# Performance work log

Measured on AMD Instinct MI355X. Metric: run time of the kernel, lower is better.

## Reference

```python
import jax, jax.numpy as jnp
import numpy as np
import math

V, D, H, KVH, L, T, B = 32000, 1024, 16, 4, 4, 2048, 2
HD = D // H            # head_dim = 64
GROUP = H // KVH       # GQA group size = 4
KVW = KVH * HD         # kv width = 256
EPS = 1e-5


def _alibi_slopes(n_heads):
    # n_heads=16 is a power of two
    start = 2.0 ** (-2.0 ** (-(math.log2(n_heads) - 3)))
    return np.array([start * start ** i for i in range(n_heads)], dtype=np.float32)


def setup_inputs() -> dict:
    key = jax.random.key(0)
    ks = jax.random.split(key, 8)
    s = 0.02
    inp = {
        "tok_emb": jax.random.normal(ks[0], (V, D), jnp.float32) * s,
        "ln1_s": jnp.ones((L, D), jnp.float32),
        "ln1_b": jnp.zeros((L, D), jnp.float32),
        "qkv_w": jax.random.normal(ks[1], (L, D, D + 2 * KVW), jnp.float32) * s,
        "qkv_b": jnp.zeros((L, D + 2 * KVW), jnp.float32),
        "proj_w": jax.random.normal(ks[2], (L, D, D), jnp.float32) * s,
        "proj_b": jnp.zeros((L, D), jnp.float32),
        "ln2_s": jnp.ones((L, D), jnp.float32),
        "ln2_b": jnp.zeros((L, D), jnp.float32),
        "fc1_w": jax.random.normal(ks[3], (L, D, 4 * D), jnp.float32) * s,
        "fc1_b": jnp.zeros((L, 4 * D), jnp.float32),
        "fc2_w": jax.random.normal(ks[4], (L, 4 * D, D), jnp.float32) * s,
        "fc2_b": jnp.zeros((L, D), jnp.float32),
        "lnf_s": jnp.ones((D,), jnp.float32),
        "lnf_b": jnp.zeros((D,), jnp.float32),
        "idx": jax.random.randint(ks[5], (B, T), 0, V, jnp.int32),
    }
    return inp


def _ln(x, s, b):
    mu = jnp.mean(x, axis=-1, keepdims=True)
    var = jnp.var(x, axis=-1, keepdims=True)
    return (x - mu) * jax.lax.rsqrt(var + EPS) * s + b


def _forward(tok_emb, ln1_s, ln1_b, qkv_w, qkv_b, proj_w, proj_b,
             ln2_s, ln2_b, fc1_w, fc1_b, fc2_w, fc2_b, lnf_s, lnf_b, idx):
    x = tok_emb[idx]  # (B, T, D); ALiBi => no learned positional embedding

    # combined causal mask + ALiBi bias: (1, H, T, T)
    slopes = jnp.asarray(_alibi_slopes(H)).reshape(1, H, 1, 1)
    pos = jnp.arange(T, dtype=jnp.float32)
    rel = jnp.minimum(pos[None, :] - pos[:, None], 0.0)  # (T, T), clamp_max(0)
    causal = pos[None, :] <= pos[:, None]
    bias = jnp.where(causal[None, None], rel[None, None] * slopes, -jnp.inf)

    scale = 1.0 / math.sqrt(HD)
    for l in range(L):
        h = _ln(x, ln1_s[l], ln1_b[l])
        qkv = h @ qkv_w[l] + qkv_b[l]
        q = qkv[..., :D].reshape(B, T, H, HD).transpose(0, 2, 1, 3)
        k = qkv[..., D:D + KVW].reshape(B, T, KVH, HD).transpose(0, 2, 1, 3)
        v = qkv[..., D + KVW:].reshape(B, T, KVH, HD).transpose(0, 2, 1, 3)
        k = jnp.repeat(k, GROUP, axis=1)  # GQA broadcast -> (B, H, T, HD)
        v = jnp.repeat(v, GROUP, axis=1)
        att = jnp.einsum("bhqd,bhkd->bhqk", q, k) * scale + bias
        att = jax.nn.softmax(att, axis=-1)
        o = jnp.einsum("bhqk,bhkd->bhqd", att, v)
        o = o.transpose(0, 2, 1, 3).reshape(B, T, D)
        x = x + o @ proj_w[l] + proj_b[l]
        h = _ln(x, ln2_s[l], ln2_b[l])
        x = x + jax.nn.gelu(h @ fc1_w[l] + fc1_b[l], approximate=False) @ fc2_w[l] + fc2_b[l]

    x = _ln(x, lnf_s, lnf_b)
    logits = x @ tok_emb.T  # tied head (no bias)
    return logits


def reference(tok_emb, ln1_s, ln1_b, qkv_w, qkv_b, proj_w, proj_b,
              ln2_s, ln2_b, fc1_w, fc1_b, fc2_w, fc2_b, lnf_s, lnf_b, idx):
    return _forward(tok_emb, ln1_s, ln1_b, qkv_w, qkv_b, proj_w, proj_b,
                    ln2_s, ln2_b, fc1_w, fc1_b, fc2_w, fc2_b, lnf_s, lnf_b, idx)
```

## Files before the change

### kernel.cpp

```cpp
#include <hip/hip_runtime.h>

#define DEV __device__ __forceinline__
typedef unsigned short u16;
typedef __bf16 bf16_t;
typedef bf16_t bf16x8 __attribute__((ext_vector_type(8)));
typedef float f32x4 __attribute__((ext_vector_type(4)));

DEV u16 f2bf(float f){ unsigned u=__float_as_uint(f); return (u16)((u + 0x7fffu + ((u>>16)&1u))>>16); }

DEV void gl_lds16(const void* g, void* l){
  __builtin_amdgcn_global_load_lds((__attribute__((address_space(1))) void*)g,
                                   (__attribute__((address_space(3))) void*)l, 16, 0, 0);
}
DEV f32x4 MFMA(bf16x8 a, bf16x8 b, f32x4 c){
  return __builtin_amdgcn_mfma_f32_16x16x32_bf16(a, b, c, 0, 0, 0);
}
DEV bf16x8 ld8(const u16* p){ return *(const bf16x8*)p; }

__global__ __launch_bounds__(256) void k_embed(const int* __restrict__ idx,
                                               const float* __restrict__ emb,
                                               float* __restrict__ x){
  int row = blockIdx.x;
  int tok = idx[row];
  const float4* s = (const float4*)(emb + (size_t)tok*1024);
  float4* d = (float4*)(x + (size_t)row*1024);
  d[threadIdx.x] = s[threadIdx.x];
}

__global__ __launch_bounds__(256) void k_ln(const float* __restrict__ x,
                                            const float* __restrict__ sc,
                                            const float* __restrict__ bi,
                                            u16* __restrict__ out){
  int row = blockIdx.x;
  const float* xr = x + (size_t)row*1024;
  float4 v = ((const float4*)xr)[threadIdx.x];
  float s = v.x+v.y+v.z+v.w;
  float q = v.x*v.x+v.y*v.y+v.z*v.z+v.w*v.w;
  #pragma unroll
  for(int m=1;m<64;m<<=1){ s += __shfl_xor(s,m); q += __shfl_xor(q,m); }
  __shared__ float ss[4], sq[4];
  int w = threadIdx.x>>6;
  if((threadIdx.x&63)==0){ ss[w]=s; sq[w]=q; }
  __syncthreads();
  s = ss[0]+ss[1]+ss[2]+ss[3];
  q = sq[0]+sq[1]+sq[2]+sq[3];
  float mu = s*(1.f/1024.f);
  float var = q*(1.f/1024.f) - mu*mu;
  float rs = rsqrtf(var + 1e-5f);
  float4 sv = ((const float4*)sc)[threadIdx.x];
  float4 bv = ((const float4*)bi)[threadIdx.x];
  ushort4 o;
  o.x = f2bf((v.x-mu)*rs*sv.x + bv.x);
  o.y = f2bf((v.y-mu)*rs*sv.y + bv.y);
  o.z = f2bf((v.z-mu)*rs*sv.z + bv.z);
  o.w = f2bf((v.w-mu)*rs*sv.w + bv.w);
  *(ushort4*)(out + (size_t)row*1024 + threadIdx.x*4) = o;
}

__global__ __launch_bounds__(256) void k_convT(const float* __restrict__ W,
                                               u16* __restrict__ Wt, int K, int N){
  __shared__ float tile[32][33];
  size_t loff = (size_t)blockIdx.z * K * N;
  W  += loff;  Wt += loff;
  int n0 = blockIdx.x*32, k0 = blockIdx.y*32;
  int tx = threadIdx.x & 31, ty = threadIdx.x >> 5;
  #pragma unroll
  for(int i=0;i<4;i++)
    tile[ty + i*8][tx] = W[(size_t)(k0 + ty + i*8)*N + n0 + tx];
  __syncthreads();
  #pragma unroll
  for(int i=0;i<4;i++)
    Wt[(size_t)(n0 + ty + i*8)*K + k0 + tx] = f2bf(tile[tx][ty + i*8]);
}

__global__ __launch_bounds__(256) void k_conv(const float* __restrict__ in,
                                              u16* __restrict__ out, int n4){
  int i = blockIdx.x*256 + threadIdx.x;
  if(i < n4){
    float4 v = ((const float4*)in)[i];
    ushort4 o; o.x=f2bf(v.x); o.y=f2bf(v.y); o.z=f2bf(v.z); o.w=f2bf(v.w);
    ((ushort4*)out)[i] = o;
  }
}

template<int EPI, int SWAP>
__global__ __launch_bounds__(256) void k_gemm(const u16* __restrict__ A,
                                              const u16* __restrict__ Bt,
                                              const float* __restrict__ bias,
                                              void* __restrict__ out,
                                              float* __restrict__ res,
                                              int M, int N, int K, int m_base){
  __shared__ __align__(16) u16 As[128*64];
  __shared__ __align__(16) u16 Bs[128*64];
  int t = threadIdx.x, l = t & 63, w = t >> 6;
  int g = l >> 4, lr = l & 15;
  int wr = w >> 1, wc = w & 1;
  int m0, n0;
  if constexpr(SWAP){ m0 = m_base + blockIdx.x*128; n0 = blockIdx.y*128; }
  else              { m0 = m_base + blockIdx.y*128; n0 = blockIdx.x*128; }
  f32x4 acc[4][4];
  #pragma unroll
  for(int i=0;i<4;i++)
    #pragma unroll
    for(int j=0;j<4;j++) acc[i][j] = f32x4{0.f,0.f,0.f,0.f};

  int sr = t >> 3;
  int sc = (((t & 7) ^ (sr & 7)) * 8);
  const u16* pa = A  + (size_t)(m0 + sr)*K + sc;
  const u16* pb = Bt + (size_t)(n0 + sr)*K + sc;
  u16* lda = As + t*8;
  u16* ldb = Bs + t*8;
  const int rs_a = (lr & 7)*8;

  for(int k0=0; k0<K; k0+=64){
    #pragma unroll
    for(int i=0;i<4;i++){
      gl_lds16(pa + (size_t)(i*32)*K, lda + i*2048);
      gl_lds16(pb + (size_t)(i*32)*K, ldb + i*2048);
    }
    pa += 64; pb += 64;
    __syncthreads();
    bf16x8 af[4][2], bfr[4][2];
    #pragma unroll
    for(int mi=0;mi<4;mi++){
      int row = wr*64 + mi*16 + lr;
      af[mi][0] = ld8(&As[row*64 + ((g*8     ) ^ rs_a)]);
      af[mi][1] = ld8(&As[row*64 + ((g*8 + 32) ^ rs_a)]);
    }
    #pragma unroll
    for(int ni=0;ni<4;ni++){
      int row = wc*64 + ni*16 + lr;
      bfr[ni][0] = ld8(&Bs[row*64 + ((g*8     ) ^ rs_a)]);
      bfr[ni][1] = ld8(&Bs[row*64 + ((g*8 + 32) ^ rs_a)]);
    }
    #pragma unroll
    for(int mi=0;mi<4;mi++)
      #pragma unroll
      for(int ni=0;ni<4;ni++){
        acc[mi][ni] = MFMA(af[mi][0], bfr[ni][0], acc[mi][ni]);
        acc[mi][ni] = MFMA(af[mi][1], bfr[ni][1], acc[mi][ni]);
      }
    __syncthreads();
  }

  float bv[4];
  #pragma unroll
  for(int ni=0;ni<4;ni++){
    if constexpr(EPI==3) bv[ni] = 0.f;
    else bv[ni] = bias[n0 + wc*64 + ni*16 + lr];
  }
  #pragma unroll
  for(int mi=0;mi<4;mi++){
    int row = m0 + wr*64 + mi*16 + g*4;
    #pragma unroll
    for(int ni=0;ni<4;ni++){
      int col = n0 + wc*64 + ni*16 + lr;
      #pragma unroll
      for(int r=0;r<4;r++){
        float v = acc[mi][ni][r] + bv[ni];
        size_t oidx = (size_t)(row + r)*N + col;
        if constexpr(EPI==0){
          ((u16*)out)[oidx] = f2bf(v);
        } else if constexpr(EPI==1){
          res[oidx] += v;
        } else if constexpr(EPI==2){
          float gv = 0.5f*v*(1.f + erff(v*0.70710678118654752f));
          ((u16*)out)[oidx] = f2bf(gv);
        } else {
          ((float*)out)[oidx] = v;
        }
      }
    }
  }
}

__global__ __launch_bounds__(256) void k_gemm_f32b(const u16* __restrict__ A,
                                                   const float* __restrict__ B,
                                                   float* __restrict__ out,
                                                   int M, int N, int K, int m_base){
  __shared__ __align__(16) u16 As[128*32];
  __shared__ __align__(16) u16 Bs[128*32];
  int t = threadIdx.x, l = t & 63, w = t >> 6;
  int g = l >> 4, lr = l & 15;
  int wr = w >> 1, wc = w & 1;
  int m0 = m_base + blockIdx.y*128, n0 = blockIdx.x*128;
  f32x4 acc[4][4];
  #pragma unroll
  for(int i=0;i<4;i++)
    #pragma unroll
    for(int j=0;j<4;j++) acc[i][j] = f32x4{0.f,0.f,0.f,0.f};

  int r0 = t >> 2, c0 = (t & 3)*8;
  const u16* pa0 = A + (size_t)(m0 + r0)*K + c0;
  const u16* pa1 = A + (size_t)(m0 + r0 + 64)*K + c0;
  u16* la0 = As + t*8;  u16* la1 = As + (t+256)*8;
  int br = t >> 1, bc = (t & 1)*16;
  const float* pb = B + (size_t)(n0 + br)*K + bc;

  for(int k0=0; k0<K; k0+=32){
    gl_lds16(pa0, la0); gl_lds16(pa1, la1);
    pa0 += 32; pa1 += 32;
    float4 f0 = ((const float4*)pb)[0];
    float4 f1 = ((const float4*)pb)[1];
    float4 f2 = ((const float4*)pb)[2];
    float4 f3 = ((const float4*)pb)[3];
    pb += 32;
    ushort4 u0{f2bf(f0.x),f2bf(f0.y),f2bf(f0.z),f2bf(f0.w)};
    ushort4 u1{f2bf(f1.x),f2bf(f1.y),f2bf(f1.z),f2bf(f1.w)};
    ushort4 u2{f2bf(f2.x),f2bf(f2.y),f2bf(f2.z),f2bf(f2.w)};
    ushort4 u3{f2bf(f3.x),f2bf(f3.y),f2bf(f3.z),f2bf(f3.w)};
    *(ushort4*)&Bs[br*32 + bc +  0] = u0;
    *(ushort4*)&Bs[br*32 + bc +  4] = u1;
    *(ushort4*)&Bs[br*32 + bc +  8] = u2;
    *(ushort4*)&Bs[br*32 + bc + 12] = u3;
    __syncthreads();
    bf16x8 af[4], bfr[4];
    #pragma unroll
    for(int mi=0;mi<4;mi++) af[mi]  = ld8(&As[(wr*64 + mi*16 + lr)*32 + g*8]);
    #pragma unroll
    for(int ni=0;ni<4;ni++) bfr[ni] = ld8(&Bs[(wc*64 + ni*16 + lr)*32 + g*8]);
    #pragma unroll
    for(int mi=0;mi<4;mi++)
      #pragma unroll
      for(int ni=0;ni<4;ni++)
        acc[mi][ni] = MFMA(af[mi], bfr[ni], acc[mi][ni]);
    __syncthreads();
  }

  #pragma unroll
  for(int mi=0;mi<4;mi++){
    int row = m0 + wr*64 + mi*16 + g*4;
    #pragma unroll
    for(int ni=0;ni<4;ni++){
      int col = n0 + wc*64 + ni*16 + lr;
      #pragma unroll
      for(int r=0;r<4;r++)
        out[(size_t)(row + r)*N + col] = acc[mi][ni][r];
    }
  }
}

__global__ __launch_bounds__(256) void k_attn(const u16* __restrict__ qkv,
                                              u16* __restrict__ atto){
  __shared__ __align__(16) u16 Ksm[64*72];
  __shared__ __align__(16) u16 Vsm[64*72];
  __shared__ __align__(16) u16 Psm[4][16*72];
  int t = threadIdx.x, l = t & 63, w = t >> 6, g = l >> 4, lr = l & 15;
  int bh = blockIdx.y; int b = bh >> 4, h = bh & 15, kvh = h >> 2;
  int qb = blockIdx.x * 64;
  const float L2E = 1.44269504088896f;
  const float C1  = 0.125f * L2E;
  float slopeL = exp2f(-0.5f*(float)(h+1)) * L2E;
  float sLkt[4];
  #pragma unroll
  for(int kt=0;kt<4;kt++) sLkt[kt] = slopeL*(float)(kt*16+lr);

  int qrow = qb + w*16 + lr;
  const u16* qp = qkv + (size_t)(b*2048 + qrow)*1536 + h*64;
  bf16x8 qf0 = ld8(qp + g*8);
  bf16x8 qf1 = ld8(qp + 32 + g*8);

  bf16_t onev = (bf16_t)1.0f;
  bf16x8 onesb = {onev,onev,onev,onev,onev,onev,onev,onev};

  f32x4 oacc[4];
  #pragma unroll
  for(int i=0;i<4;i++) oacc[i] = f32x4{0.f,0.f,0.f,0.f};
  f32x4 lsum = f32x4{0.f,0.f,0.f,0.f};

  int nkb = blockIdx.x + 1;
  for(int kb=0; kb<nkb; kb++){
    __syncthreads();
    #pragma unroll
    for(int i=0;i<2;i++){
      int tt = t + i*256;
      int key = tt >> 3, ho = (tt & 7)*8;
      const u16* src = qkv + (size_t)(b*2048 + kb*64 + key)*1536 + 1024 + kvh*64 + ho;
      *(int4*)&Ksm[key*72 + ho] = *(const int4*)src;
    }
    {
      int key0 = (t>>3)*2, hd0 = (t&7)*8;
      const u16* v0 = qkv + (size_t)(b*2048 + kb*64 + key0)*1536 + 1280 + kvh*64 + hd0;
      int4 A0 = *(const int4*)v0;
      int4 A1 = *(const int4*)(v0 + 1536);
      const u16* ua = (const u16*)&A0; const u16* ub = (const u16*)&A1;
      #pragma unroll
      for(int j=0;j<8;j++){
        int row = hd0 + j;
        int colp = key0 ^ ((row>>3)*8);
        unsigned pr = (unsigned)ua[j] | ((unsigned)ub[j]<<16);
        *(unsigned*)&Vsm[row*72 + colp] = pr;
      }
    }
    __syncthreads();
    f32x4 sacc[4];
    #pragma unroll
    for(int kt=0;kt<4;kt++) sacc[kt] = f32x4{0.f,0.f,0.f,0.f};
    #pragma unroll
    for(int kt=0;kt<4;kt++){
      bf16x8 kf0 = ld8(&Ksm[(kt*16+lr)*72 + g*8]);
      bf16x8 kf1 = ld8(&Ksm[(kt*16+lr)*72 + 32 + g*8]);
      sacc[kt] = MFMA(qf0, kf0, sacc[kt]);
      sacc[kt] = MFMA(qf1, kf1, sacc[kt]);
    }
    #pragma unroll
    for(int r=0;r<4;r++){
      int q = qb + w*16 + g*4 + r;
      float base = slopeL*(float)(kb*64 - q) - 8.0f*L2E;
      #pragma unroll
      for(int kt=0;kt<4;kt++){
        int key = kb*64 + kt*16 + lr;
        float f = fmaf(sacc[kt][r], C1, base + sLkt[kt]);
        float p = (key <= q) ? exp2f(f) : 0.f;
        Psm[w][(g*4+r)*72 + kt*16 + lr] = f2bf(p);
      }
    }
    #pragma unroll
    for(int ks=0;ks<2;ks++){
      bf16x8 pf = ld8(&Psm[w][lr*72 + ks*32 + g*8]);
      lsum = MFMA(pf, onesb, lsum);
      #pragma unroll
      for(int ht=0;ht<4;ht++){
        int row = ht*16 + lr;
        int colp = (ks*32 + g*8) ^ ((row>>3)*8);
        bf16x8 vf = ld8(&Vsm[row*72 + colp]);
        oacc[ht] = MFMA(pf, vf, oacc[ht]);
      }
    }
  }
  #pragma unroll
  for(int ht=0;ht<4;ht++){
    #pragma unroll
    for(int r=0;r<4;r++){
      float o = oacc[ht][r] / lsum[r];
      atto[(size_t)(b*2048 + qb + w*16 + g*4 + r)*1024 + h*64 + ht*16 + lr] = f2bf(o);
    }
  }
}

extern "C" void kernel_launch(void* const* d_in, const int* in_sizes, int n_in,
                              void* d_out, int out_size, void* d_ws, size_t ws_size,
                              hipStream_t stream) {
  const float* tok_emb = (const float*)d_in[0];
  const float* ln1_s   = (const float*)d_in[1];
  const float* ln1_b   = (const float*)d_in[2];
  const float* qkv_w   = (const float*)d_in[3];
  const float* qkv_b   = (const float*)d_in[4];
  const float* proj_w  = (const float*)d_in[5];
  const float* proj_b  = (const float*)d_in[6];
  const float* ln2_s   = (const float*)d_in[7];
  const float* ln2_b   = (const float*)d_in[8];
  const float* fc1_w   = (const float*)d_in[9];
  const float* fc1_b   = (const float*)d_in[10];
  const float* fc2_w   = (const float*)d_in[11];
  const float* fc2_b   = (const float*)d_in[12];
  const float* lnf_s   = (const float*)d_in[13];
  const float* lnf_b   = (const float*)d_in[14];
  const int*   idx     = (const int*)d_in[15];

  char* ob = (char*)d_out;
  float* xf32  = (float*)(ob);
  u16* qkv_bf  = (u16*)(ob + (size_t)16777216);
  u16* atto_bf = (u16*)(ob + (size_t)29360128);
  u16* mid_bf  = (u16*)(ob + (size_t)37748736);
  u16* wt_qkv  = (u16*)(ob + (size_t)71303168);
  u16* wt_proj = (u16*)(ob + (size_t)83886080);
  u16* wt_fc1  = (u16*)(ob + (size_t)92274688);
  u16* wt_fc2  = (u16*)(ob + (size_t)125829120);
  u16* h_bf    = (u16*)d_ws;
  float* out   = (float*)d_out;

  bool big_ws = ws_size >= (size_t)(8388608 + 65536000);
  u16* te_bf = big_ws ? (u16*)((char*)d_ws + 8388608)
                      : (u16*)(ob + (size_t)294912000);

  k_conv<<<32000, 256, 0, stream>>>(tok_emb, te_bf, 8192000);
  k_embed<<<4096, 256, 0, stream>>>(idx, tok_emb, xf32);
  k_convT<<<dim3(48,32,4), 256, 0, stream>>>(qkv_w,  wt_qkv, 1024, 1536);
  k_convT<<<dim3(32,32,4), 256, 0, stream>>>(proj_w, wt_proj, 1024, 1024);
  k_convT<<<dim3(128,32,4), 256, 0, stream>>>(fc1_w, wt_fc1, 1024, 4096);
  k_convT<<<dim3(32,128,4), 256, 0, stream>>>(fc2_w, wt_fc2, 4096, 1024);

  for(int l=0; l<4; l++){
    k_ln<<<4096, 256, 0, stream>>>(xf32, ln1_s + (size_t)l*1024, ln1_b + (size_t)l*1024, h_bf);
    k_gemm<0,0><<<dim3(12,32), 256, 0, stream>>>(h_bf, wt_qkv + (size_t)l*1536*1024,
                                                 qkv_b + (size_t)l*1536,
                                                 qkv_bf, nullptr, 4096, 1536, 1024, 0);
    k_attn<<<dim3(32,32), 256, 0, stream>>>(qkv_bf, atto_bf);
    k_gemm<1,0><<<dim3(8,32), 256, 0, stream>>>(atto_bf, wt_proj + (size_t)l*1024*1024,
                                                proj_b + (size_t)l*1024,
                                                nullptr, xf32, 4096, 1024, 1024, 0);
    k_ln<<<4096, 256, 0, stream>>>(xf32, ln2_s + (size_t)l*1024, ln2_b + (size_t)l*1024, h_bf);
    k_gemm<2,0><<<dim3(32,32), 256, 0, stream>>>(h_bf, wt_fc1 + (size_t)l*4096*1024,
                                                 fc1_b + (size_t)l*4096,
                                                 mid_bf, nullptr, 4096, 4096, 1024, 0);
    k_gemm<1,0><<<dim3(8,32), 256, 0, stream>>>(mid_bf, wt_fc2 + (size_t)l*1024*4096,
                                                fc2_b + (size_t)l*1024,
                                                nullptr, xf32, 4096, 1024, 4096, 0);
  }
  k_ln<<<4096, 256, 0, stream>>>(xf32, lnf_s, lnf_b, h_bf);

  if(big_ws){
    k_gemm<3,1><<<dim3(32,250), 256, 0, stream>>>(h_bf, te_bf, nullptr, out, nullptr,
                                                  4096, 32000, 1024, 0);
  } else {
    k_gemm<3,1><<<dim3(18,250), 256, 0, stream>>>(h_bf, te_bf, nullptr, out, nullptr,
                                                  4096, 32000, 1024, 0);
    k_gemm<3,1><<<dim3(10,250), 256, 0, stream>>>(h_bf, te_bf, nullptr, out, nullptr,
                                                  4096, 32000, 1024, 2816);
    k_gemm_f32b<<<dim3(250,4), 256, 0, stream>>>(h_bf, tok_emb, out,
                                                 4096, 32000, 1024, 2304);
  }
}
```

Baseline: 1.729 ms.

## Add 256x256-tile double-buffered GEMM for the tied LM-head projection

Adds a new 512-thread GEMM kernel with 256x256 output tiles and K-step 64. It double-buffers A and B in LDS through direct global-to-LDS loads and uses an XOR swizzle, overlapping the prefetch of the next K tile with MFMA work on the current one through staged barriers and priority hints. The LM-head logits GEMM now launches this kernel in place of the 128x128 kernel, aiming for more data reuse per load and better latency hiding on the largest GEMM. It uses 128KB of LDS per block, which limits occupancy to one block per CU, and it relies on hand-tuned waitcnt counts.

Result: no change. 1.718 ms (-0.6%).

```diff
diff --git a/kernel.cpp b/kernel.cpp
--- a/kernel.cpp
+++ b/kernel.cpp
@@ -170,6 +170,104 @@
           ((float*)out)[oidx] = v;
         }
       }
+    }
+  }
+}
+
+__global__ __launch_bounds__(512) void k_gemm256(const u16* __restrict__ A,
+                                                 const u16* __restrict__ Bt,
+                                                 float* __restrict__ out,
+                                                 int M, int N, int K, int m_base){
+  __shared__ __align__(16) u16 As[2][256*64];
+  __shared__ __align__(16) u16 Bs[2][256*64];
+  int t = threadIdx.x, l = t & 63, wid = t >> 6;
+  int g = l >> 4, lr = l & 15;
+  int m0 = m_base + blockIdx.x*256, n0 = blockIdx.y*256;
+  f32x4 acc[2][16];
+  #pragma unroll
+  for(int mi=0;mi<2;mi++)
+    #pragma unroll
+    for(int i=0;i<16;i++) acc[mi][i] = f32x4{0.f,0.f,0.f,0.f};
+
+  int srow = t >> 3;
+  int scol = ((t & 7) ^ (srow & 7)) * 8;
+  const int rs = (lr & 7) * 8;
+  int nt = K >> 6;
+
+  auto stage_half = [&](int jj, int h){
+    int buf = jj & 1; int k0s = jj << 6;
+    if(h < 2){
+      #pragma unroll
+      for(int c=0;c<2;c++){
+        int rr = h*128 + c*64 + srow;
+        gl_lds16(A + (size_t)(m0 + rr)*K + k0s + scol,
+                 &As[buf][rr*64 + (t&7)*8]);
+      }
+    } else {
+      #pragma unroll
+      for(int c=0;c<2;c++){
+        int rr = (h-2)*128 + c*64 + srow;
+        gl_lds16(Bt + (size_t)(n0 + rr)*K + k0s + scol,
+                 &Bs[buf][rr*64 + (t&7)*8]);
+      }
+    }
+  };
+
+  stage_half(0,0); stage_half(0,1); stage_half(0,2); stage_half(0,3);
+  asm volatile("s_waitcnt vmcnt(2)" ::: "memory");
+  __builtin_amdgcn_s_barrier();
+  __builtin_amdgcn_sched_barrier(0);
+
+  bf16x8 af[2][2];
+  for(int j=0; j<nt; ++j){
+    const u16* Ab = As[j & 1];
+    const u16* Bb = Bs[j & 1];
+    bool pf = (j + 1 < nt);
+    #pragma unroll
+    for(int q=0; q<4; ++q){
+      if(q == 0){
+        #pragma unroll
+        for(int mi=0;mi<2;mi++){
+          int row = wid*32 + mi*16 + lr;
+          af[mi][0] = ld8(&Ab[row*64 + ((g*8     ) ^ rs)]);
+          af[mi][1] = ld8(&Ab[row*64 + ((g*8 + 32) ^ rs)]);
+        }
+      }
+      bf16x8 bfr[4][2];
+      #pragma unroll
+      for(int i=0;i<4;i++){
+        int row = (q*4 + i)*16 + lr;
+        bfr[i][0] = ld8(&Bb[row*64 + ((g*8     ) ^ rs)]);
+        bfr[i][1] = ld8(&Bb[row*64 + ((g*8 + 32) ^ rs)]);
+      }
+      if(pf) stage_half(j+1, q);
+      __builtin_amdgcn_s_barrier();
+      __builtin_amdgcn_sched_barrier(0);
+      __builtin_amdgcn_s_setprio(1);
+      #pragma unroll
+      for(int mi=0;mi<2;mi++)
+        #pragma unroll
+        for(int i=0;i<4;i++){
+          acc[mi][q*4+i] = MFMA(af[mi][0], bfr[i][0], acc[mi][q*4+i]);
+          acc[mi][q*4+i] = MFMA(af[mi][1], bfr[i][1], acc[mi][q*4+i]);
+        }
+      __builtin_amdgcn_s_setprio(0);
+      if(q == 1) asm volatile("s_waitcnt vmcnt(4)" ::: "memory");
+      if(q == 3) asm volatile("s_waitcnt vmcnt(2)" ::: "memory");
+      __builtin_amdgcn_s_barrier();
+      __builtin_amdgcn_sched_barrier(0);
+    }
+  }
+
+  #pragma unroll
+  for(int mi=0;mi<2;mi++){
+    int row = m0 + wid*32 + mi*16 + g*4;
+    #pragma unroll
+    for(int i=0;i<16;i++){
+      int col = n0 + i*16 + lr;
+      #pragma unroll
+      for(int r=0;r<4;r++)
+        out[(size_t)(row + r)*N + col] = acc[mi][i][r];
     }
   }
 }
@@ -401,13 +499,13 @@
   k_ln<<<4096, 256, 0, stream>>>(xf32, lnf_s, lnf_b, h_bf);
 
   if(big_ws){
-    k_gemm<3,1><<<dim3(32,250), 256, 0, stream>>>(h_bf, te_bf, nullptr, out, nullptr,
-                                                  4096, 32000, 1024, 0);
+    k_gemm256<<<dim3(16,125), 512, 0, stream>>>(h_bf, te_bf, out,
+                                                4096, 32000, 1024, 0);
   } else {
-    k_gemm<3,1><<<dim3(18,250), 256, 0, stream>>>(h_bf, te_bf, nullptr, out, nullptr,
-                                                  4096, 32000, 1024, 0);
-    k_gemm<3,1><<<dim3(10,250), 256, 0, stream>>>(h_bf, te_bf, nullptr, out, nullptr,
-                                                  4096, 32000, 1024, 2816);
+    k_gemm256<<<dim3(9,125), 512, 0, stream>>>(h_bf, te_bf, out,
+                                               4096, 32000, 1024, 0);
+    k_gemm256<<<dim3(5,125), 512, 0, stream>>>(h_bf, te_bf, out,
+                                               4096, 32000, 1024, 2816);
     k_gemm_f32b<<<dim3(250,4), 256, 0, stream>>>(h_bf, tok_emb, out,
                                                  4096, 32000, 1024, 2304);
   }
```
